# Optimization experiments

Hardware: AMD Instinct MI355X
Metric: run time of the kernel (lower is better)

## Reference

```python
import jax, jax.numpy as jnp
import numpy as np

B, S, H = 2, 2048, 2048
NH, HD = 16, 128


def rotate_half(x):
    x1, x2 = x[..., : x.shape[-1] // 2], x[..., x.shape[-1] // 2 :]
    return jnp.concatenate((-x2, x1), axis=-1)


def setup_inputs() -> dict:
    key = jax.random.key(0)
    ks = jax.random.split(key, 8)
    return {
        "hidden": jax.random.normal(ks[0], (B, S, H), dtype=jnp.float32),
        "cos": jax.random.uniform(ks[1], (S, HD), dtype=jnp.float32),
        "sin": jax.random.uniform(ks[2], (S, HD), dtype=jnp.float32),
        "attention_mask": jnp.zeros((B, 1, S, S), dtype=jnp.float32),
        "Wq": jax.random.normal(ks[3], (H, H), dtype=jnp.float32) * 0.02,
        "Wk": jax.random.normal(ks[4], (H, H), dtype=jnp.float32) * 0.02,
        "Wv": jax.random.normal(ks[5], (H, H), dtype=jnp.float32) * 0.02,
        "Wo": jax.random.normal(ks[6], (H, H), dtype=jnp.float32) * 0.02,
    }


def reference(hidden, cos, sin, attention_mask, Wq, Wk, Wv, Wo):
    b, s, h = hidden.shape
    # torch Linear: y = x @ W.T ; reshape to [B, NH, S, HD]
    def proj(W):
        return (hidden @ W.T).reshape(b, s, NH, HD).transpose(0, 2, 1, 3)

    q, k, v = proj(Wq), proj(Wk), proj(Wv)
    c = cos[None, None, :, :]  # [1,1,S,HD]
    si = sin[None, None, :, :]
    q = q * c + rotate_half(q) * si
    k = k * c + rotate_half(k) * si
    scores = jnp.einsum("bhqd,bhkd->bhqk", q, k) / jnp.sqrt(jnp.float32(HD))
    scores = scores + attention_mask
    attn = jax.nn.softmax(scores.astype(jnp.float32), axis=-1).astype(q.dtype)
    out = jnp.einsum("bhqk,bhkd->bhqd", attn, v)
    out = out.transpose(0, 2, 1, 3).reshape(b, s, h)
    return out @ Wo.T
```

## Files before the change

### kernel.cpp

```cpp
#include <hip/hip_runtime.h>
#include <hip/hip_bf16.h>
#include <math.h>

#define SEQ 2048
#define HID 2048
#define NHEAD 16
#define HDIM 128
#define LDK 4096

typedef __bf16 bf16_t;
typedef __bf16 bf16x2 __attribute__((ext_vector_type(2)));
typedef __bf16 bf16x4_t __attribute__((ext_vector_type(4)));
typedef __bf16 bf16x8 __attribute__((ext_vector_type(8)));
typedef float f32x4 __attribute__((ext_vector_type(4)));
typedef float f32x16 __attribute__((ext_vector_type(16)));
typedef unsigned u32x4 __attribute__((ext_vector_type(4)));

#define MFMA16(a, b, c) __builtin_amdgcn_mfma_f32_16x16x32_bf16(a, b, c, 0, 0, 0)
#define MFMA32(a, b, c) __builtin_amdgcn_mfma_f32_32x32x16_bf16(a, b, c, 0, 0, 0)
#define GLOAD_LDS(g, l) \
  __builtin_amdgcn_global_load_lds((const __attribute__((address_space(1))) void*)(g), \
                                   (__attribute__((address_space(3))) void*)(l), 16, 0, 0)

static __device__ inline unsigned pk2(float lo, float hi) {
  bf16x2 t; t[0] = (bf16_t)lo; t[1] = (bf16_t)hi;
  return __builtin_bit_cast(unsigned, t);
}

__global__ void cast_hidden(const float* __restrict__ in, bf16_t* __restrict__ out) {
  int i = blockIdx.x * 256 + threadIdx.x;
  float4 v = ((const float4*)in)[i];
  bf16x4_t b;
  b[0] = (bf16_t)v.x; b[1] = (bf16_t)v.y; b[2] = (bf16_t)v.z; b[3] = (bf16_t)v.w;
  ((bf16x4_t*)out)[i] = b;
}

__global__ void cast_weights(const float* __restrict__ a, const float* __restrict__ b,
                             const float* __restrict__ c, const float* __restrict__ d,
                             bf16_t* __restrict__ out) {
  const float* srcs[4] = {a, b, c, d};
  const float* src = srcs[blockIdx.y];
  bf16_t* dst = out + (size_t)blockIdx.y * (HID * HID);
  int i = blockIdx.x * 256 + threadIdx.x;
  float4 v = ((const float4*)src)[i];
  bf16x4_t o;
  o[0] = (bf16_t)v.x; o[1] = (bf16_t)v.y; o[2] = (bf16_t)v.z; o[3] = (bf16_t)v.w;
  ((bf16x4_t*)dst)[i] = o;
}

__global__ __launch_bounds__(512, 2) void gemm256(
    const bf16_t* __restrict__ A, const bf16_t* __restrict__ Bw,
    bf16_t* __restrict__ Cb, float* __restrict__ Cf, int M, int N, int K) {
  __shared__ char smem[131072];
  const int tid = threadIdx.x, lane = tid & 63, wid = tid >> 6;
  const int wr = wid >> 2, wc = wid & 3;
  const int lr = lane & 15, lg = lane >> 4;
  const int xcd = blockIdx.x & 7, l = blockIdx.x >> 3;
  const int brow = (xcd >> 2) * 8 + (l >> 2);
  const int bcol = (xcd & 3) * 4 + (l & 3);
  const int NT = K >> 6;

  const bf16_t* Ab = A + (size_t)(brow * 256) * K;
  const bf16_t* Bb = Bw + (size_t)(bcol * 256) * K;

  f32x4 acc[8][4] = {};
  bf16x8 af[4], bfr[4];
  const int swz = (lg ^ ((lr >> 1) & 3)) << 4;

#define STAGE_HALF(t_, op, kh)                                                        \
  {                                                                                   \
    int tt = (t_) < NT ? (t_) : NT - 1;                                               \
    const bf16_t* gsrc = (op) ? Bb : Ab;                                              \
    char* ldst = smem + (tt & 1) * 65536 + (op) * 32768 + (kh) * 16384;               \
    _Pragma("unroll") for (int is = 0; is < 2; ++is) {                                \
      int p = tid + is * 512;                                                         \
      int row = p >> 2, ch = p & 3;                                                   \
      GLOAD_LDS(gsrc + (size_t)row * K + tt * 64 + (kh) * 32 +                        \
                    ((ch ^ ((row >> 1) & 3)) * 8),                                    \
                ldst + p * 16);                                                       \
    }                                                                                 \
  }

#define PHASE(cb, kh, mh, LOADB, STAGECALL, VM)                                       \
  {                                                                                   \
    _Pragma("unroll") for (int mf = 0; mf < 4; ++mf) {                                \
      int row = wr * 128 + (mh) * 64 + mf * 16 + lr;                                  \
      af[mf] = *(const bf16x8*)(smem + (cb) * 65536 + (kh) * 16384 + row * 64 + swz); \
    }                                                                                 \
    if (LOADB) {                                                                      \
      _Pragma("unroll") for (int nf = 0; nf < 4; ++nf) {                              \
        int row = wc * 64 + nf * 16 + lr;                                             \
        bfr[nf] = *(const bf16x8*)(smem + (cb) * 65536 + 32768 + (kh) * 16384 +       \
                                   row * 64 + swz);                                   \
      }                                                                               \
    }                                                                                 \
    STAGECALL;                                                                        \
    __builtin_amdgcn_s_barrier();                                                     \
    asm volatile("s_waitcnt lgkmcnt(0)" ::: "memory");                                \
    __builtin_amdgcn_sched_barrier(0);                                                \
    __builtin_amdgcn_s_setprio(1);                                                    \
    _Pragma("unroll") for (int mf = 0; mf < 4; ++mf)                                  \
      _Pragma("unroll") for (int nf = 0; nf < 4; ++nf)                                \
        acc[(mh) * 4 + mf][nf] = MFMA16(af[mf], bfr[nf], acc[(mh) * 4 + mf][nf]);     \
    __builtin_amdgcn_s_setprio(0);                                                    \
    if (VM) { asm volatile("s_waitcnt vmcnt(6)" ::: "memory"); }                      \
    __builtin_amdgcn_s_barrier();                                                     \
    __builtin_amdgcn_sched_barrier(0);                                                \
  }

  STAGE_HALF(0, 1, 0); STAGE_HALF(0, 0, 0); STAGE_HALF(0, 1, 1); STAGE_HALF(0, 0, 1);
  STAGE_HALF(1, 1, 0); STAGE_HALF(1, 0, 0); STAGE_HALF(1, 1, 1);
  asm volatile("s_waitcnt vmcnt(6)" ::: "memory");
  __builtin_amdgcn_s_barrier();
  __builtin_amdgcn_sched_barrier(0);

  const int NI = NT >> 1;
  for (int i = 0; i < NI; ++i) {
    const int t2 = 2 * i;
    PHASE(0, 0, 0, 1, STAGE_HALF(t2 + 1, 0, 1), 0);
    PHASE(0, 0, 1, 0, STAGE_HALF(t2 + 2, 1, 0), 0);
    PHASE(0, 1, 0, 1, STAGE_HALF(t2 + 2, 0, 0), 0);
    PHASE(0, 1, 1, 0, STAGE_HALF(t2 + 2, 1, 1), 1);
    PHASE(1, 0, 0, 1, STAGE_HALF(t2 + 2, 0, 1), 0);
    PHASE(1, 0, 1, 0, STAGE_HALF(t2 + 3, 1, 0), 0);
    PHASE(1, 1, 0, 1, STAGE_HALF(t2 + 3, 0, 0), 0);
    PHASE(1, 1, 1, 0, STAGE_HALF(t2 + 3, 1, 1), 1);
  }
#undef PHASE
#undef STAGE_HALF

#pragma unroll
  for (int mi = 0; mi < 8; ++mi)
#pragma unroll
    for (int nf = 0; nf < 4; ++nf)
#pragma unroll
      for (int r = 0; r < 4; ++r) {
        int row = brow * 256 + wr * 128 + (mi >> 2) * 64 + (mi & 3) * 16 + lg * 4 + r;
        int col = bcol * 256 + wc * 64 + nf * 16 + lr;
        float v = acc[mi][nf][r];
        if (Cf) Cf[(size_t)row * N + col] = v;
        else    Cb[(size_t)row * N + col] = (bf16_t)v;
      }
}

__global__ __launch_bounds__(256, 3) void gemm_bt(
    const bf16_t* __restrict__ A, const bf16_t* __restrict__ Bw,
    bf16_t* __restrict__ Cb, float* __restrict__ Cf,
    int M, int N, int K) {
  __shared__ bf16_t As[2][128 * 32];
  __shared__ bf16_t Bs[2][128 * 32];
  const int tid = threadIdx.x;
  const int lane = tid & 63, wid = tid >> 6;
  const int wr = wid >> 1, wc = wid & 1;
  const int lr = lane & 15, lg = lane >> 4;
  const int nwg = gridDim.x;
  const int lid = (blockIdx.x & 7) * (nwg >> 3) + (blockIdx.x >> 3);
  const int nbc = N >> 7;
  const int brow = lid / nbc, bcol = lid % nbc;

  f32x4 acc[4][4] = {};
  const int swz = lg ^ ((lr >> 1) & 3);

  const int srow = tid >> 2, sch = tid & 3;
#define GSTAGE(k0, bb)                                                                   \
  {                                                                                      \
    _Pragma("unroll") for (int is = 0; is < 2; ++is) {                                   \
      int row = srow + is * 64;                                                          \
      int g = (sch ^ ((row >> 1) & 3)) * 8;                                              \
      GLOAD_LDS(A + (size_t)(brow * 128 + row) * K + (k0) + g,                           \
                &As[bb][(row * 4 + sch) * 8]);                                           \
      GLOAD_LDS(Bw + (size_t)(bcol * 128 + row) * K + (k0) + g,                          \
                &Bs[bb][(row * 4 + sch) * 8]);                                           \
    }                                                                                    \
  }

  GSTAGE(0, 0);
  __syncthreads();

  const int nt = K / 32;
  for (int t = 0; t < nt; ++t) {
    const int cb = t & 1;
    if (t + 1 < nt) GSTAGE((t + 1) * 32, cb ^ 1);
    bf16x8 af[4], bfr[4];
#pragma unroll
    for (int m = 0; m < 4; ++m)
      af[m] = *(const bf16x8*)(&As[cb][(wr * 64 + m * 16 + lr) * 32 + swz * 8]);
#pragma unroll
    for (int n = 0; n < 4; ++n)
      bfr[n] = *(const bf16x8*)(&Bs[cb][(wc * 64 + n * 16 + lr) * 32 + swz * 8]);
#pragma unroll
    for (int m = 0; m < 4; ++m)
#pragma unroll
      for (int n = 0; n < 4; ++n)
        acc[m][n] = MFMA16(af[m], bfr[n], acc[m][n]);
    __syncthreads();
  }
#undef GSTAGE

#pragma unroll
  for (int m = 0; m < 4; ++m)
#pragma unroll
    for (int n = 0; n < 4; ++n)
#pragma unroll
      for (int r = 0; r < 4; ++r) {
        int row = brow * 128 + wr * 64 + m * 16 + lg * 4 + r;
        int col = bcol * 128 + wc * 64 + n * 16 + lr;
        float v = acc[m][n][r];
        if (Cf) Cf[(size_t)row * N + col] = v;
        else    Cb[(size_t)row * N + col] = (bf16_t)v;
      }
}

__global__ void rope_qk(bf16_t* __restrict__ QK,
                        const float* __restrict__ cost, const float* __restrict__ sint) {
  const float SCALE = 0.08838834764831845f;
  int idx = blockIdx.x * 256 + threadIdx.x;
  int d8 = idx & 7;
  int t = idx >> 3;
  int h = t & 15;
  int row = t >> 4;
  int s = row & (SEQ - 1);
  size_t base = (size_t)row * LDK + h * HDIM;
  const float4* cp = (const float4*)(cost + s * HDIM);
  const float4* sp = (const float4*)(sint + s * HDIM);
  float4 c0a = cp[d8 * 2], c0b = cp[d8 * 2 + 1];
  float4 c1a = cp[16 + d8 * 2], c1b = cp[16 + d8 * 2 + 1];
  float4 s0a = sp[d8 * 2], s0b = sp[d8 * 2 + 1];
  float4 s1a = sp[16 + d8 * 2], s1b = sp[16 + d8 * 2 + 1];
  float c0[8] = {c0a.x, c0a.y, c0a.z, c0a.w, c0b.x, c0b.y, c0b.z, c0b.w};
  float c1[8] = {c1a.x, c1a.y, c1a.z, c1a.w, c1b.x, c1b.y, c1b.z, c1b.w};
  float s0[8] = {s0a.x, s0a.y, s0a.z, s0a.w, s0b.x, s0b.y, s0b.z, s0b.w};
  float s1[8] = {s1a.x, s1a.y, s1a.z, s1a.w, s1b.x, s1b.y, s1b.z, s1b.w};

  bf16_t* Q = QK;
  bf16_t* K = QK + 2048;
  bf16x8 qlo = *(bf16x8*)(Q + base + d8 * 8);
  bf16x8 qhi = *(bf16x8*)(Q + base + 64 + d8 * 8);
  bf16x8 klo = *(bf16x8*)(K + base + d8 * 8);
  bf16x8 khi = *(bf16x8*)(K + base + 64 + d8 * 8);
  bf16x8 qlo2, qhi2, klo2, khi2;
#pragma unroll
  for (int j = 0; j < 8; ++j) {
    float q0 = (float)qlo[j], q1 = (float)qhi[j];
    qlo2[j] = (bf16_t)((q0 * c0[j] - q1 * s0[j]) * SCALE);
    qhi2[j] = (bf16_t)((q1 * c1[j] + q0 * s1[j]) * SCALE);
    float k0 = (float)klo[j], k1 = (float)khi[j];
    klo2[j] = (bf16_t)(k0 * c0[j] - k1 * s0[j]);
    khi2[j] = (bf16_t)(k1 * c1[j] + k0 * s1[j]);
  }
  *(bf16x8*)(Q + base + d8 * 8) = qlo2;
  *(bf16x8*)(Q + base + 64 + d8 * 8) = qhi2;
  *(bf16x8*)(K + base + d8 * 8) = klo2;
  *(bf16x8*)(K + base + 64 + d8 * 8) = khi2;
}

__global__ void transpose_v(const bf16_t* __restrict__ Vf, bf16_t* __restrict__ Vt) {
  __shared__ bf16_t t[32][33];
  int tx = threadIdx.x & 31, ty = threadIdx.x >> 5;
  int r0 = blockIdx.y * 32, c0 = blockIdx.x * 32;
#pragma unroll
  for (int j = 0; j < 4; ++j)
    t[ty + j * 8][tx] = Vf[(size_t)(r0 + ty + j * 8) * HID + c0 + tx];
  __syncthreads();
#pragma unroll
  for (int j = 0; j < 4; ++j) {
    int c = c0 + ty + j * 8;
    int r = r0 + tx;
    int h = c >> 7, d = c & 127, b = r >> 11, s = r & (SEQ - 1);
    Vt[(((size_t)(b * NHEAD + h)) * HDIM + d) * SEQ + s] = t[tx][ty + j * 8];
  }
}

__global__ void mask_t(const float* __restrict__ m, bf16_t* __restrict__ mt) {
  __shared__ float t[32][33];
  int tx = threadIdx.x & 31, ty = threadIdx.x >> 5;
  int r0 = blockIdx.y * 32, c0 = blockIdx.x * 32;
  const float* mb = m + (size_t)blockIdx.z * SEQ * SEQ;
  bf16_t* mtb = mt + (size_t)blockIdx.z * SEQ * SEQ;
#pragma unroll
  for (int j = 0; j < 4; ++j)
    t[ty + j * 8][tx] = mb[(size_t)(r0 + ty + j * 8) * SEQ + c0 + tx];
  __syncthreads();
#pragma unroll
  for (int j = 0; j < 4; ++j)
    mtb[(size_t)(c0 + ty + j * 8) * SEQ + r0 + tx] = (bf16_t)t[tx][ty + j * 8];
}

__global__ __launch_bounds__(512, 2) void flash_fwd(
    const bf16_t* __restrict__ Qf, const bf16_t* __restrict__ Kf,
    const bf16_t* __restrict__ Vt, const bf16_t* __restrict__ maskT,
    bf16_t* __restrict__ AO) {
  __shared__ char smem[131072];
  char* KsB = smem;
  char* VsB = smem + 65536;
  const int tid = threadIdx.x, lane = tid & 63, wid = tid >> 6;
  const int q32 = lane & 31, hi = lane >> 5;

  const int x = blockIdx.x;
  const int bh = x & 31, qt = x >> 5;
  const int b = bh >> 4, h = bh & 15;
  const int qg = qt * 256 + wid * 32 + q32;

  bf16x8 qf[8];
  const bf16_t* qptr = Qf + (size_t)(b * SEQ + qg) * LDK + h * HDIM + hi * 8;
#pragma unroll
  for (int ds = 0; ds < 8; ++ds) qf[ds] = *(const bf16x8*)(qptr + ds * 16);

  const bf16_t* mQ = maskT + (size_t)b * SEQ * SEQ + qg;

  float mrun = -INFINITY, lpart = 0.f;
  f32x16 o[4] = {};

#define STAGE_KV(kt_, bb)                                                                \
  {                                                                                      \
    const int kb0_ = (kt_) * 128;                                                        \
    _Pragma("unroll") for (int is = 0; is < 4; ++is) {                                   \
      int p = tid + is * 512;                                                            \
      int row = p >> 4, ch = p & 15;                                                     \
      int src = (ch * 16) ^ ((row & 7) << 4);                                            \
      GLOAD_LDS((const char*)(Kf + (size_t)(b * SEQ + kb0_ + row) * LDK + h * HDIM) +    \
                    src,                                                                 \
                KsB + (bb) * 32768 + p * 16);                                            \
      GLOAD_LDS((const char*)(Vt + (size_t)(bh * HDIM + row) * SEQ + kb0_) + src,        \
                VsB + (bb) * 32768 + p * 16);                                            \
    }                                                                                    \
  }

  STAGE_KV(0, 0);
  __syncthreads();

  const int NT = SEQ / 128;
  for (int kt = 0; kt < NT; ++kt) {
    const int cur = kt & 1;
    const int kb0 = kt * 128;
    if (kt + 1 < NT) STAGE_KV(kt + 1, cur ^ 1);

#pragma unroll
    for (int kb = 0; kb < 4; ++kb) {
      f32x16 sacc;
#pragma unroll
      for (int r = 0; r < 16; ++r) {
        int key = kb0 + kb * 32 + (r & 3) + 8 * (r >> 2) + 4 * hi;
        sacc[r] = (float)mQ[(size_t)key * SEQ];
      }
#pragma unroll
      for (int ds = 0; ds < 8; ++ds) {
        int row = kb * 32 + q32;
        bf16x8 kfr = *(const bf16x8*)(KsB + cur * 32768 + row * 256 +
                                      ((ds * 32 + hi * 16) ^ ((row & 7) << 4)));
        sacc = MFMA32(kfr, qf[ds], sacc);
      }

      float mx = sacc[0];
#pragma unroll
      for (int r = 1; r < 16; ++r) mx = fmaxf(mx, sacc[r]);
      mx = fmaxf(mx, __shfl_xor(mx, 32, 64));
      if (!__all(mx <= mrun + 8.f)) {
        float mnew = fmaxf(mrun, mx);
        float corr = __expf(mrun - mnew);
        mrun = mnew;
        lpart *= corr;
#pragma unroll
        for (int d0 = 0; d0 < 4; ++d0)
#pragma unroll
          for (int r = 0; r < 16; ++r) o[d0][r] *= corr;
      }

      float p[16];
      float rs = 0.f;
#pragma unroll
      for (int r = 0; r < 16; ++r) {
        p[r] = __expf(sacc[r] - mrun);
        rs += p[r];
      }
      lpart += rs;

#pragma unroll
      for (int s = 0; s < 2; ++s) {
        unsigned A1 = pk2(p[8 * s + 0], p[8 * s + 1]);
        unsigned A2 = pk2(p[8 * s + 2], p[8 * s + 3]);
        unsigned B1 = pk2(p[8 * s + 4], p[8 * s + 5]);
        unsigned B2 = pk2(p[8 * s + 6], p[8 * s + 7]);
        unsigned A1s = __shfl_xor(A1, 32, 64);
        unsigned A2s = __shfl_xor(A2, 32, 64);
        unsigned B1s = __shfl_xor(B1, 32, 64);
        unsigned B2s = __shfl_xor(B2, 32, 64);
        unsigned w0 = hi ? B1s : A1;
        unsigned w1 = hi ? B2s : A2;
        unsigned w2 = hi ? B1 : A1s;
        unsigned w3 = hi ? B2 : A2s;
        u32x4 W = {w0, w1, w2, w3};
        bf16x8 pav = __builtin_bit_cast(bf16x8, W);
        const int gs = kb * 2 + s;
#pragma unroll
        for (int d0 = 0; d0 < 4; ++d0) {
          int vrow = d0 * 32 + q32;
          bf16x8 vf = *(const bf16x8*)(VsB + cur * 32768 + vrow * 256 +
                                       ((gs * 32 + hi * 16) ^ ((vrow & 7) << 4)));
          o[d0] = MFMA32(vf, pav, o[d0]);
        }
      }
    }
    __syncthreads();
  }
#undef STAGE_KV

  float l = lpart + __shfl_xor(lpart, 32, 64);
  float rl = 1.f / l;
  bf16_t* aorow = AO + (size_t)(b * SEQ + qg) * HID + h * HDIM;
#pragma unroll
  for (int d0 = 0; d0 < 4; ++d0)
#pragma unroll
    for (int g = 0; g < 4; ++g) {
      unsigned lo = pk2(o[d0][4 * g + 0] * rl, o[d0][4 * g + 1] * rl);
      unsigned hi2 = pk2(o[d0][4 * g + 2] * rl, o[d0][4 * g + 3] * rl);
      int d = d0 * 32 + 8 * g + 4 * hi;
      *(unsigned*)(aorow + d) = lo;
      *(unsigned*)(aorow + d + 2) = hi2;
    }
}

extern "C" void kernel_launch(void* const* d_in, const int* in_sizes, int n_in,
                              void* d_out, int out_size, void* d_ws, size_t ws_size,
                              hipStream_t stream) {
  const float* hidden = (const float*)d_in[0];
  const float* cost   = (const float*)d_in[1];
  const float* sint   = (const float*)d_in[2];
  const float* mask   = (const float*)d_in[3];
  const float* Wq     = (const float*)d_in[4];
  const float* Wk     = (const float*)d_in[5];
  const float* Wv     = (const float*)d_in[6];
  const float* Wo     = (const float*)d_in[7];
  float* out = (float*)d_out;
  char* ws = (char*)d_ws;

  bf16_t* Af    = (bf16_t*)(ws + 0);
  bf16_t* Wqb   = (bf16_t*)(ws + 16777216);
  bf16_t* Wvb   = (bf16_t*)(ws + 33554432);
  bf16_t* Wob   = (bf16_t*)(ws + 41943040);
  bf16_t* QK    = (bf16_t*)(ws + 50331648);
  bf16_t* Vf    = (bf16_t*)(ws + 83886080);
  bf16_t* Vt    = (bf16_t*)(ws + 0);
  bf16_t* maskT = (bf16_t*)(ws + 83886080);
  bf16_t* AO    = (bf16_t*)(ws + 16777216);

  cast_hidden<<<8192, 256, 0, stream>>>(hidden, Af);
  cast_weights<<<dim3(4096, 4), 256, 0, stream>>>(Wq, Wk, Wv, Wo, Wqb);

  gemm256<<<256, 512, 0, stream>>>(Af, Wqb, QK, nullptr, 4096, LDK, HID);
  gemm_bt<<<512, 256, 0, stream>>>(Af, Wvb, Vf, nullptr, 4096, HID, HID);

  rope_qk<<<2048, 256, 0, stream>>>(QK, cost, sint);
  transpose_v<<<dim3(64, 128), 256, 0, stream>>>(Vf, Vt);
  mask_t<<<dim3(64, 64, 2), 256, 0, stream>>>(mask, maskT);

  flash_fwd<<<256, 512, 0, stream>>>(QK, QK + 2048, Vt, maskT, AO);

  gemm_bt<<<512, 256, 0, stream>>>(AO, Wob, nullptr, out, 4096, HID, HID);
}
```

Measured before the change: 319.0 us.

## Pack mask into MFMA-fragment layout and shrink flash tiles to 128x64

Replaces the transposed mask with a packed layout that matches the MFMA accumulator fragment, so each lane loads its 16 mask values as two contiguous 16-byte vectors instead of 16 strided scalar loads. The flash kernel moves to 256-thread blocks covering 128 queries with 64-key tiles and half the LDS, doubling the grid to 512 blocks for better occupancy and CU coverage. Max and sum reductions are rewritten as trees to shorten dependency chains. Smaller key tiles mean more barriers and more K/V staging rounds per block.

```diff
diff --git a/kernel.cpp b/kernel.cpp
--- a/kernel.cpp
+++ b/kernel.cpp
@@ -271,89 +271,103 @@
   }
 }
 
-__global__ void mask_t(const float* __restrict__ m, bf16_t* __restrict__ mt) {
+__global__ void mask_pack(const float* __restrict__ m, bf16_t* __restrict__ mp) {
   __shared__ float t[32][33];
   int tx = threadIdx.x & 31, ty = threadIdx.x >> 5;
-  int r0 = blockIdx.y * 32, c0 = blockIdx.x * 32;
+  int q0 = blockIdx.x * 32, k0 = blockIdx.y * 32;
   const float* mb = m + (size_t)blockIdx.z * SEQ * SEQ;
-  bf16_t* mtb = mt + (size_t)blockIdx.z * SEQ * SEQ;
 #pragma unroll
   for (int j = 0; j < 4; ++j)
-    t[ty + j * 8][tx] = mb[(size_t)(r0 + ty + j * 8) * SEQ + c0 + tx];
+    t[ty + j * 8][tx] = mb[(size_t)(q0 + ty + j * 8) * SEQ + k0 + tx];
   __syncthreads();
-#pragma unroll
-  for (int j = 0; j < 4; ++j)
-    mtb[(size_t)(c0 + ty + j * 8) * SEQ + r0 + tx] = (bf16_t)t[tx][ty + j * 8];
-}
-
-__global__ __launch_bounds__(512, 2) void flash_fwd(
+  int r = tx & 15, hi = tx >> 4;
+  int kl = (r & 3) + 8 * (r >> 2) + 4 * hi;
+  bf16_t* ob = mp + ((size_t)(blockIdx.z * 64 + blockIdx.y) * 2048 + q0) * 32;
+#pragma unroll
+  for (int j = 0; j < 4; ++j) {
+    int qloc = ty + j * 8;
+    ob[(size_t)qloc * 32 + tx] = (bf16_t)t[qloc][kl];
+  }
+}
+
+__global__ __launch_bounds__(256, 2) void flash_fwd(
     const bf16_t* __restrict__ Qf, const bf16_t* __restrict__ Kf,
-    const bf16_t* __restrict__ Vt, const bf16_t* __restrict__ maskT,
+    const bf16_t* __restrict__ Vt, const bf16_t* __restrict__ maskP,
     bf16_t* __restrict__ AO) {
-  __shared__ char smem[131072];
+  __shared__ char smem[65536];
   char* KsB = smem;
-  char* VsB = smem + 65536;
+  char* VsB = smem + 32768;
   const int tid = threadIdx.x, lane = tid & 63, wid = tid >> 6;
   const int q32 = lane & 31, hi = lane >> 5;
 
   const int x = blockIdx.x;
   const int bh = x & 31, qt = x >> 5;
   const int b = bh >> 4, h = bh & 15;
-  const int qg = qt * 256 + wid * 32 + q32;
+  const int qg = qt * 128 + wid * 32 + q32;
 
   bf16x8 qf[8];
   const bf16_t* qptr = Qf + (size_t)(b * SEQ + qg) * LDK + h * HDIM + hi * 8;
 #pragma unroll
   for (int ds = 0; ds < 8; ++ds) qf[ds] = *(const bf16x8*)(qptr + ds * 16);
 
-  const bf16_t* mQ = maskT + (size_t)b * SEQ * SEQ + qg;
+  const bf16_t* mQ = maskP + (size_t)b * 64 * 65536 + (size_t)qg * 32 + hi * 16;
 
   float mrun = -INFINITY, lpart = 0.f;
   f32x16 o[4] = {};
 
 #define STAGE_KV(kt_, bb)                                                                \
   {                                                                                      \
-    const int kb0_ = (kt_) * 128;                                                        \
+    const int kb0_ = (kt_) * 64;                                                         \
     _Pragma("unroll") for (int is = 0; is < 4; ++is) {                                   \
-      int p = tid + is * 512;                                                            \
+      int p = tid + is * 256;                                                            \
       int row = p >> 4, ch = p & 15;                                                     \
       int src = (ch * 16) ^ ((row & 7) << 4);                                            \
       GLOAD_LDS((const char*)(Kf + (size_t)(b * SEQ + kb0_ + row) * LDK + h * HDIM) +    \
                     src,                                                                 \
-                KsB + (bb) * 32768 + p * 16);                                            \
-      GLOAD_LDS((const char*)(Vt + (size_t)(bh * HDIM + row) * SEQ + kb0_) + src,        \
-                VsB + (bb) * 32768 + p * 16);                                            \
+                KsB + (bb) * 16384 + p * 16);                                            \
+    }                                                                                    \
+    _Pragma("unroll") for (int is = 0; is < 4; ++is) {                                   \
+      int p = tid + is * 256;                                                            \
+      int vrow = p >> 3, vch = p & 7;                                                    \
+      int vsrc = (vch * 16) ^ ((vrow & 7) << 4);                                         \
+      GLOAD_LDS((const char*)(Vt + (size_t)(bh * HDIM + vrow) * SEQ + kb0_) + vsrc,      \
+                VsB + (bb) * 16384 + p * 16);                                            \
     }                                                                                    \
   }
 
   STAGE_KV(0, 0);
   __syncthreads();
 
-  const int NT = SEQ / 128;
+  const int NT = SEQ / 64;
   for (int kt = 0; kt < NT; ++kt) {
     const int cur = kt & 1;
-    const int kb0 = kt * 128;
     if (kt + 1 < NT) STAGE_KV(kt + 1, cur ^ 1);
 
 #pragma unroll
-    for (int kb = 0; kb < 4; ++kb) {
+    for (int kb = 0; kb < 2; ++kb) {
+      const int kg = kt * 2 + kb;
+      bf16x8 mk0 = *(const bf16x8*)(mQ + (size_t)kg * 65536);
+      bf16x8 mk1 = *(const bf16x8*)(mQ + (size_t)kg * 65536 + 8);
       f32x16 sacc;
 #pragma unroll
-      for (int r = 0; r < 16; ++r) {
-        int key = kb0 + kb * 32 + (r & 3) + 8 * (r >> 2) + 4 * hi;
-        sacc[r] = (float)mQ[(size_t)key * SEQ];
-      }
+      for (int r = 0; r < 8; ++r) sacc[r] = (float)mk0[r];
+#pragma unroll
+      for (int r = 0; r < 8; ++r) sacc[8 + r] = (float)mk1[r];
+
 #pragma unroll
       for (int ds = 0; ds < 8; ++ds) {
         int row = kb * 32 + q32;
-        bf16x8 kfr = *(const bf16x8*)(KsB + cur * 32768 + row * 256 +
+        bf16x8 kfr = *(const bf16x8*)(KsB + cur * 16384 + row * 256 +
                                       ((ds * 32 + hi * 16) ^ ((row & 7) << 4)));
         sacc = MFMA32(kfr, qf[ds], sacc);
       }
 
-      float mx = sacc[0];
-#pragma unroll
-      for (int r = 1; r < 16; ++r) mx = fmaxf(mx, sacc[r]);
+      float a0 = fmaxf(sacc[0], sacc[1]),  a1 = fmaxf(sacc[2], sacc[3]);
+      float a2 = fmaxf(sacc[4], sacc[5]),  a3 = fmaxf(sacc[6], sacc[7]);
+      float a4 = fmaxf(sacc[8], sacc[9]),  a5 = fmaxf(sacc[10], sacc[11]);
+      float a6 = fmaxf(sacc[12], sacc[13]), a7 = fmaxf(sacc[14], sacc[15]);
+      float mx = fmaxf(fmaxf(fmaxf(a0, a1), fmaxf(a2, a3)),
+                       fmaxf(fmaxf(a4, a5), fmaxf(a6, a7)));
       mx = fmaxf(mx, __shfl_xor(mx, 32, 64));
       if (!__all(mx <= mrun + 8.f)) {
         float mnew = fmaxf(mrun, mx);
@@ -367,13 +381,13 @@
       }
 
       float p[16];
-      float rs = 0.f;
-#pragma unroll
-      for (int r = 0; r < 16; ++r) {
-        p[r] = __expf(sacc[r] - mrun);
-        rs += p[r];
-      }
-      lpart += rs;
+#pragma unroll
+      for (int r = 0; r < 16; ++r) p[r] = __expf(sacc[r] - mrun);
+      {
+        float s0 = p[0] + p[1],  s1 = p[2] + p[3],  s2 = p[4] + p[5],  s3 = p[6] + p[7];
+        float s4 = p[8] + p[9],  s5 = p[10] + p[11], s6 = p[12] + p[13], s7 = p[14] + p[15];
+        lpart += ((s0 + s1) + (s2 + s3)) + ((s4 + s5) + (s6 + s7));
+      }
 
 #pragma unroll
       for (int s = 0; s < 2; ++s) {
@@ -395,7 +409,7 @@
 #pragma unroll
         for (int d0 = 0; d0 < 4; ++d0) {
           int vrow = d0 * 32 + q32;
-          bf16x8 vf = *(const bf16x8*)(VsB + cur * 32768 + vrow * 256 +
+          bf16x8 vf = *(const bf16x8*)(VsB + cur * 16384 + vrow * 128 +
                                        ((gs * 32 + hi * 16) ^ ((vrow & 7) << 4)));
           o[d0] = MFMA32(vf, pav, o[d0]);
         }
@@ -441,7 +455,7 @@
   bf16_t* QK    = (bf16_t*)(ws + 50331648);
   bf16_t* Vf    = (bf16_t*)(ws + 83886080);
   bf16_t* Vt    = (bf16_t*)(ws + 0);
-  bf16_t* maskT = (bf16_t*)(ws + 83886080);
+  bf16_t* maskP = (bf16_t*)(ws + 83886080);
   bf16_t* AO    = (bf16_t*)(ws + 16777216);
 
   cast_hidden<<<8192, 256, 0, stream>>>(hidden, Af);
@@ -452,9 +466,9 @@
 
   rope_qk<<<2048, 256, 0, stream>>>(QK, cost, sint);
   transpose_v<<<dim3(64, 128), 256, 0, stream>>>(Vf, Vt);
-  mask_t<<<dim3(64, 64, 2), 256, 0, stream>>>(mask, maskT);
-
-  flash_fwd<<<256, 512, 0, stream>>>(QK, QK + 2048, Vt, maskT, AO);
+  mask_pack<<<dim3(64, 64, 2), 256, 0, stream>>>(mask, maskP);
+
+  flash_fwd<<<512, 256, 0, stream>>>(QK, QK + 2048, Vt, maskP, AO);
 
   gemm_bt<<<512, 256, 0, stream>>>(AO, Wob, nullptr, out, 4096, HID, HID);
 }
```

Result: no change. 321.8 us (+0.9%).

## Process two query tiles per wave and pre-pack mask into MFMA layout

Applied to the files above, without the earlier changes.

The flash attention kernel now uses 256 threads per block, with each wave handling 64 query rows as two 32-row MFMA tiles. Each K and V fragment read from LDS is reused across both tiles, halving LDS reads per MFMA. The mask is repacked by a new kernel into a layout matching the MFMA accumulator, so it loads with vector reads instead of 16 strided scalar loads per tile. The LDS swizzle widens to 16 rows. In exchange, register pressure roughly doubles and occupancy drops to one 4-wave block per CU, which may expose latency.

```diff
diff --git a/kernel.cpp b/kernel.cpp
--- a/kernel.cpp
+++ b/kernel.cpp
@@ -25,6 +25,23 @@
 static __device__ inline unsigned pk2(float lo, float hi) {
   bf16x2 t; t[0] = (bf16_t)lo; t[1] = (bf16_t)hi;
   return __builtin_bit_cast(unsigned, t);
+}
+
+static __device__ inline bf16x8 pack_slice(const float* p, int hi) {
+  unsigned A1 = pk2(p[0], p[1]);
+  unsigned A2 = pk2(p[2], p[3]);
+  unsigned B1 = pk2(p[4], p[5]);
+  unsigned B2 = pk2(p[6], p[7]);
+  unsigned A1s = __shfl_xor(A1, 32, 64);
+  unsigned A2s = __shfl_xor(A2, 32, 64);
+  unsigned B1s = __shfl_xor(B1, 32, 64);
+  unsigned B2s = __shfl_xor(B2, 32, 64);
+  unsigned w0 = hi ? B1s : A1;
+  unsigned w1 = hi ? B2s : A2;
+  unsigned w2 = hi ? B1 : A1s;
+  unsigned w3 = hi ? B2 : A2s;
+  u32x4 W = {w0, w1, w2, w3};
+  return __builtin_bit_cast(bf16x8, W);
 }
 
 __global__ void cast_hidden(const float* __restrict__ in, bf16_t* __restrict__ out) {
@@ -271,24 +288,28 @@
   }
 }
 
-__global__ void mask_t(const float* __restrict__ m, bf16_t* __restrict__ mt) {
+__global__ void mask_pack(const float* __restrict__ m, bf16_t* __restrict__ mp) {
   __shared__ float t[32][33];
   int tx = threadIdx.x & 31, ty = threadIdx.x >> 5;
-  int r0 = blockIdx.y * 32, c0 = blockIdx.x * 32;
+  int q0 = blockIdx.x * 32, k0 = blockIdx.y * 32;
   const float* mb = m + (size_t)blockIdx.z * SEQ * SEQ;
-  bf16_t* mtb = mt + (size_t)blockIdx.z * SEQ * SEQ;
 #pragma unroll
   for (int j = 0; j < 4; ++j)
-    t[ty + j * 8][tx] = mb[(size_t)(r0 + ty + j * 8) * SEQ + c0 + tx];
+    t[ty + j * 8][tx] = mb[(size_t)(q0 + ty + j * 8) * SEQ + k0 + tx];
   __syncthreads();
-#pragma unroll
-  for (int j = 0; j < 4; ++j)
-    mtb[(size_t)(c0 + ty + j * 8) * SEQ + r0 + tx] = (bf16_t)t[tx][ty + j * 8];
-}
-
-__global__ __launch_bounds__(512, 2) void flash_fwd(
+  int r = tx & 15, hi = tx >> 4;
+  int kl = (r & 3) + 8 * (r >> 2) + 4 * hi;
+  bf16_t* ob = mp + ((size_t)(blockIdx.z * 64 + blockIdx.y) * 2048 + q0) * 32;
+#pragma unroll
+  for (int j = 0; j < 4; ++j) {
+    int qloc = ty + j * 8;
+    ob[(size_t)qloc * 32 + tx] = (bf16_t)t[qloc][kl];
+  }
+}
+
+__global__ __launch_bounds__(256, 1) void flash_fwd(
     const bf16_t* __restrict__ Qf, const bf16_t* __restrict__ Kf,
-    const bf16_t* __restrict__ Vt, const bf16_t* __restrict__ maskT,
+    const bf16_t* __restrict__ Vt, const bf16_t* __restrict__ maskP,
     bf16_t* __restrict__ AO) {
   __shared__ char smem[131072];
   char* KsB = smem;
@@ -299,25 +320,31 @@
   const int x = blockIdx.x;
   const int bh = x & 31, qt = x >> 5;
   const int b = bh >> 4, h = bh & 15;
-  const int qg = qt * 256 + wid * 32 + q32;
-
-  bf16x8 qf[8];
-  const bf16_t* qptr = Qf + (size_t)(b * SEQ + qg) * LDK + h * HDIM + hi * 8;
-#pragma unroll
-  for (int ds = 0; ds < 8; ++ds) qf[ds] = *(const bf16x8*)(qptr + ds * 16);
-
-  const bf16_t* mQ = maskT + (size_t)b * SEQ * SEQ + qg;
-
-  float mrun = -INFINITY, lpart = 0.f;
-  f32x16 o[4] = {};
+  const int qg0 = qt * 256 + wid * 64 + q32;
+
+  bf16x8 qf0[8], qf1[8];
+  const bf16_t* qp0 = Qf + (size_t)(b * SEQ + qg0) * LDK + h * HDIM + hi * 8;
+  const bf16_t* qp1 = qp0 + (size_t)32 * LDK;
+#pragma unroll
+  for (int ds = 0; ds < 8; ++ds) {
+    qf0[ds] = *(const bf16x8*)(qp0 + ds * 16);
+    qf1[ds] = *(const bf16x8*)(qp1 + ds * 16);
+  }
+
+  const bf16_t* mQ0 = maskP + (size_t)b * 64 * 65536 + (size_t)qg0 * 32 + hi * 16;
+  const bf16_t* mQ1 = mQ0 + 32 * 32;
+
+  float mrun0 = -INFINITY, lpart0 = 0.f;
+  float mrun1 = -INFINITY, lpart1 = 0.f;
+  f32x16 o0[4] = {}, o1[4] = {};
 
 #define STAGE_KV(kt_, bb)                                                                \
   {                                                                                      \
     const int kb0_ = (kt_) * 128;                                                        \
-    _Pragma("unroll") for (int is = 0; is < 4; ++is) {                                   \
-      int p = tid + is * 512;                                                            \
+    _Pragma("unroll") for (int is = 0; is < 8; ++is) {                                   \
+      int p = tid + is * 256;                                                            \
       int row = p >> 4, ch = p & 15;                                                     \
-      int src = (ch * 16) ^ ((row & 7) << 4);                                            \
+      int src = (ch * 16) ^ ((row & 15) << 4);                                           \
       GLOAD_LDS((const char*)(Kf + (size_t)(b * SEQ + kb0_ + row) * LDK + h * HDIM) +    \
                     src,                                                                 \
                 KsB + (bb) * 32768 + p * 16);                                            \
@@ -332,72 +359,101 @@
   const int NT = SEQ / 128;
   for (int kt = 0; kt < NT; ++kt) {
     const int cur = kt & 1;
-    const int kb0 = kt * 128;
     if (kt + 1 < NT) STAGE_KV(kt + 1, cur ^ 1);
 
 #pragma unroll
     for (int kb = 0; kb < 4; ++kb) {
-      f32x16 sacc;
-#pragma unroll
-      for (int r = 0; r < 16; ++r) {
-        int key = kb0 + kb * 32 + (r & 3) + 8 * (r >> 2) + 4 * hi;
-        sacc[r] = (float)mQ[(size_t)key * SEQ];
-      }
+      const int kg = kt * 4 + kb;
+      bf16x8 mk00 = *(const bf16x8*)(mQ0 + (size_t)kg * 65536);
+      bf16x8 mk01 = *(const bf16x8*)(mQ0 + (size_t)kg * 65536 + 8);
+      bf16x8 mk10 = *(const bf16x8*)(mQ1 + (size_t)kg * 65536);
+      bf16x8 mk11 = *(const bf16x8*)(mQ1 + (size_t)kg * 65536 + 8);
+      f32x16 s0, s1;
+#pragma unroll
+      for (int r = 0; r < 8; ++r) {
+        s0[r] = (float)mk00[r]; s0[8 + r] = (float)mk01[r];
+        s1[r] = (float)mk10[r]; s1[8 + r] = (float)mk11[r];
+      }
+
+      const int krow = kb * 32 + q32;
+      const int kswz = (krow & 15) << 4;
 #pragma unroll
       for (int ds = 0; ds < 8; ++ds) {
-        int row = kb * 32 + q32;
-        bf16x8 kfr = *(const bf16x8*)(KsB + cur * 32768 + row * 256 +
-                                      ((ds * 32 + hi * 16) ^ ((row & 7) << 4)));
-        sacc = MFMA32(kfr, qf[ds], sacc);
-      }
-
-      float mx = sacc[0];
-#pragma unroll
-      for (int r = 1; r < 16; ++r) mx = fmaxf(mx, sacc[r]);
-      mx = fmaxf(mx, __shfl_xor(mx, 32, 64));
-      if (!__all(mx <= mrun + 8.f)) {
-        float mnew = fmaxf(mrun, mx);
-        float corr = __expf(mrun - mnew);
-        mrun = mnew;
-        lpart *= corr;
-#pragma unroll
-        for (int d0 = 0; d0 < 4; ++d0)
-#pragma unroll
-          for (int r = 0; r < 16; ++r) o[d0][r] *= corr;
-      }
-
-      float p[16];
-      float rs = 0.f;
-#pragma unroll
-      for (int r = 0; r < 16; ++r) {
-        p[r] = __expf(sacc[r] - mrun);
-        rs += p[r];
-      }
-      lpart += rs;
-
+        bf16x8 kfr = *(const bf16x8*)(KsB + cur * 32768 + krow * 256 +
+                                      ((ds * 32 + hi * 16) ^ kswz));
+        s0 = MFMA32(kfr, qf0[ds], s0);
+        s1 = MFMA32(kfr, qf1[ds], s1);
+      }
+
+      bf16x8 pav00, pav01, pav10, pav11;
+      {
+        float a0 = fmaxf(fmaxf(s0[0], s0[1]), fmaxf(s0[2], s0[3]));
+        float a1 = fmaxf(fmaxf(s0[4], s0[5]), fmaxf(s0[6], s0[7]));
+        float a2 = fmaxf(fmaxf(s0[8], s0[9]), fmaxf(s0[10], s0[11]));
+        float a3 = fmaxf(fmaxf(s0[12], s0[13]), fmaxf(s0[14], s0[15]));
+        float mx = fmaxf(fmaxf(a0, a1), fmaxf(a2, a3));
+        mx = fmaxf(mx, __shfl_xor(mx, 32, 64));
+        if (!__all(mx <= mrun0 + 8.f)) {
+          float mnew = fmaxf(mrun0, mx);
+          float corr = __expf(mrun0 - mnew);
+          mrun0 = mnew; lpart0 *= corr;
+#pragma unroll
+          for (int d0 = 0; d0 < 4; ++d0)
+#pragma unroll
+            for (int r = 0; r < 16; ++r) o0[d0][r] *= corr;
+        }
+        float p_[16];
+#pragma unroll
+        for (int r = 0; r < 16; ++r) p_[r] = __expf(s0[r] - mrun0);
+        float t0 = (p_[0] + p_[1]) + (p_[2] + p_[3]);
+        float t1 = (p_[4] + p_[5]) + (p_[6] + p_[7]);
+        float t2 = (p_[8] + p_[9]) + (p_[10] + p_[11]);
+        float t3 = (p_[12] + p_[13]) + (p_[14] + p_[15]);
+        lpart0 += (t0 + t1) + (t2 + t3);
+        pav00 = pack_slice(p_, hi);
+        pav01 = pack_slice(p_ + 8, hi);
+      }
+      {
+        float a0 = fmaxf(fmaxf(s1[0], s1[1]), fmaxf(s1[2], s1[3]));
+        float a1 = fmaxf(fmaxf(s1[4], s1[5]), fmaxf(s1[6], s1[7]));
+        float a2 = fmaxf(fmaxf(s1[8], s1[9]), fmaxf(s1[10], s1[11]));
+        float a3 = fmaxf(fmaxf(s1[12], s1[13]), fmaxf(s1[14], s1[15]));
+        float mx = fmaxf(fmaxf(a0, a1), fmaxf(a2, a3));
+        mx = fmaxf(mx, __shfl_xor(mx, 32, 64));
+        if (!__all(mx <= mrun1 + 8.f)) {
+          float mnew = fmaxf(mrun1, mx);
+          float corr = __expf(mrun1 - mnew);
+          mrun1 = mnew; lpart1 *= corr;
+#pragma unroll
+          for (int d0 = 0; d0 < 4; ++d0)
+#pragma unroll
+            for (int r = 0; r < 16; ++r) o1[d0][r] *= corr;
+        }
+        float p_[16];
+#pragma unroll
+        for (int r = 0; r < 16; ++r) p_[r] = __expf(s1[r] - mrun1);
+        float t0 = (p_[0] + p_[1]) + (p_[2] + p_[3]);
+        float t1 = (p_[4] + p_[5]) + (p_[6] + p_[7]);
+        float t2 = (p_[8] + p_[9]) + (p_[10] + p_[11]);
+        float t3 = (p_[12] + p_[13]) + (p_[14] + p_[15]);
+        lpart1 += (t0 + t1) + (t2 + t3);
+        pav10 = pack_slice(p_, hi);
+        pav11 = pack_slice(p_ + 8, hi);
+      }
+
+      const int vswzr = q32;
 #pragma unroll
       for (int s = 0; s < 2; ++s) {
-        unsigned A1 = pk2(p[8 * s + 0], p[8 * s + 1]);
-        unsigned A2 = pk2(p[8 * s + 2], p[8 * s + 3]);
-        unsigned B1 = pk2(p[8 * s + 4], p[8 * s + 5]);
-        unsigned B2 = pk2(p[8 * s + 6], p[8 * s + 7]);
-        unsigned A1s = __shfl_xor(A1, 32, 64);
-        unsigned A2s = __shfl_xor(A2, 32, 64);
-        unsigned B1s = __shfl_xor(B1, 32, 64);
-        unsigned B2s = __shfl_xor(B2, 32, 64);
-        unsigned w0 = hi ? B1s : A1;
-        unsigned w1 = hi ? B2s : A2;
-        unsigned w2 = hi ? B1 : A1s;
-        unsigned w3 = hi ? B2 : A2s;
-        u32x4 W = {w0, w1, w2, w3};
-        bf16x8 pav = __builtin_bit_cast(bf16x8, W);
         const int gs = kb * 2 + s;
+        bf16x8 pa0 = s ? pav01 : pav00;
+        bf16x8 pa1 = s ? pav11 : pav10;
 #pragma unroll
         for (int d0 = 0; d0 < 4; ++d0) {
-          int vrow = d0 * 32 + q32;
+          int vrow = d0 * 32 + vswzr;
           bf16x8 vf = *(const bf16x8*)(VsB + cur * 32768 + vrow * 256 +
-                                       ((gs * 32 + hi * 16) ^ ((vrow & 7) << 4)));
-          o[d0] = MFMA32(vf, pav, o[d0]);
+                                       ((gs * 32 + hi * 16) ^ ((vrow & 15) << 4)));
+          o0[d0] = MFMA32(vf, pa0, o0[d0]);
+          o1[d0] = MFMA32(vf, pa1, o1[d0]);
         }
       }
     }
@@ -405,18 +461,24 @@
   }
 #undef STAGE_KV
 
-  float l = lpart + __shfl_xor(lpart, 32, 64);
-  float rl = 1.f / l;
-  bf16_t* aorow = AO + (size_t)(b * SEQ + qg) * HID + h * HDIM;
+  float l0 = lpart0 + __shfl_xor(lpart0, 32, 64);
+  float l1 = lpart1 + __shfl_xor(lpart1, 32, 64);
+  float rl0 = 1.f / l0, rl1 = 1.f / l1;
+  bf16_t* ao0 = AO + (size_t)(b * SEQ + qg0) * HID + h * HDIM;
+  bf16_t* ao1 = ao0 + (size_t)32 * HID;
 #pragma unroll
   for (int d0 = 0; d0 < 4; ++d0)
 #pragma unroll
     for (int g = 0; g < 4; ++g) {
-      unsigned lo = pk2(o[d0][4 * g + 0] * rl, o[d0][4 * g + 1] * rl);
-      unsigned hi2 = pk2(o[d0][4 * g + 2] * rl, o[d0][4 * g + 3] * rl);
       int d = d0 * 32 + 8 * g + 4 * hi;
-      *(unsigned*)(aorow + d) = lo;
-      *(unsigned*)(aorow + d + 2) = hi2;
+      unsigned lo0 = pk2(o0[d0][4 * g + 0] * rl0, o0[d0][4 * g + 1] * rl0);
+      unsigned hi0 = pk2(o0[d0][4 * g + 2] * rl0, o0[d0][4 * g + 3] * rl0);
+      *(unsigned*)(ao0 + d) = lo0;
+      *(unsigned*)(ao0 + d + 2) = hi0;
+      unsigned lo1 = pk2(o1[d0][4 * g + 0] * rl1, o1[d0][4 * g + 1] * rl1);
+      unsigned hi1 = pk2(o1[d0][4 * g + 2] * rl1, o1[d0][4 * g + 3] * rl1);
+      *(unsigned*)(ao1 + d) = lo1;
+      *(unsigned*)(ao1 + d + 2) = hi1;
     }
 }
 
@@ -441,7 +503,7 @@
   bf16_t* QK    = (bf16_t*)(ws + 50331648);
   bf16_t* Vf    = (bf16_t*)(ws + 83886080);
   bf16_t* Vt    = (bf16_t*)(ws + 0);
-  bf16_t* maskT = (bf16_t*)(ws + 83886080);
+  bf16_t* maskP = (bf16_t*)(ws + 83886080);
   bf16_t* AO    = (bf16_t*)(ws + 16777216);
 
   cast_hidden<<<8192, 256, 0, stream>>>(hidden, Af);
@@ -452,9 +514,9 @@
 
   rope_qk<<<2048, 256, 0, stream>>>(QK, cost, sint);
   transpose_v<<<dim3(64, 128), 256, 0, stream>>>(Vf, Vt);
-  mask_t<<<dim3(64, 64, 2), 256, 0, stream>>>(mask, maskT);
-
-  flash_fwd<<<256, 512, 0, stream>>>(QK, QK + 2048, Vt, maskT, AO);
+  mask_pack<<<dim3(64, 64, 2), 256, 0, stream>>>(mask, maskP);
+
+  flash_fwd<<<256, 256, 0, stream>>>(QK, QK + 2048, Vt, maskP, AO);
 
   gemm_bt<<<512, 256, 0, stream>>>(AO, Wob, nullptr, out, 4096, HID, HID);
 }
```

Measured after the change: 347.2 us. 8.9% more time.

## Pack attention mask in MFMA fragment order and widen LDS swizzle

Applied to the files above, without the earlier changes.

Replaces the transposed bf16 mask with a packed layout in which each lane's 16 mask values for a 32-key block are contiguous. The flash kernel can then read them with two 16-byte loads instead of 16 scalar strided loads. It also widens the K/V LDS XOR swizzle from 8 to 16 rows to cut bank conflicts, and rewrites the max and sum reductions as trees. The new packed layout must exactly match the MFMA accumulator ordering, so any mismatch would silently produce wrong masking.

```diff
diff --git a/kernel.cpp b/kernel.cpp
--- a/kernel.cpp
+++ b/kernel.cpp
@@ -25,6 +25,23 @@
 static __device__ inline unsigned pk2(float lo, float hi) {
   bf16x2 t; t[0] = (bf16_t)lo; t[1] = (bf16_t)hi;
   return __builtin_bit_cast(unsigned, t);
+}
+
+static __device__ inline bf16x8 pack_slice(const float* p, int hi) {
+  unsigned A1 = pk2(p[0], p[1]);
+  unsigned A2 = pk2(p[2], p[3]);
+  unsigned B1 = pk2(p[4], p[5]);
+  unsigned B2 = pk2(p[6], p[7]);
+  unsigned A1s = __shfl_xor(A1, 32, 64);
+  unsigned A2s = __shfl_xor(A2, 32, 64);
+  unsigned B1s = __shfl_xor(B1, 32, 64);
+  unsigned B2s = __shfl_xor(B2, 32, 64);
+  unsigned w0 = hi ? B1s : A1;
+  unsigned w1 = hi ? B2s : A2;
+  unsigned w2 = hi ? B1 : A1s;
+  unsigned w3 = hi ? B2 : A2s;
+  u32x4 W = {w0, w1, w2, w3};
+  return __builtin_bit_cast(bf16x8, W);
 }
 
 __global__ void cast_hidden(const float* __restrict__ in, bf16_t* __restrict__ out) {
@@ -271,24 +288,28 @@
   }
 }
 
-__global__ void mask_t(const float* __restrict__ m, bf16_t* __restrict__ mt) {
+__global__ void mask_pack(const float* __restrict__ m, bf16_t* __restrict__ mp) {
   __shared__ float t[32][33];
   int tx = threadIdx.x & 31, ty = threadIdx.x >> 5;
-  int r0 = blockIdx.y * 32, c0 = blockIdx.x * 32;
+  int q0 = blockIdx.x * 32, k0 = blockIdx.y * 32;
   const float* mb = m + (size_t)blockIdx.z * SEQ * SEQ;
-  bf16_t* mtb = mt + (size_t)blockIdx.z * SEQ * SEQ;
 #pragma unroll
   for (int j = 0; j < 4; ++j)
-    t[ty + j * 8][tx] = mb[(size_t)(r0 + ty + j * 8) * SEQ + c0 + tx];
+    t[ty + j * 8][tx] = mb[(size_t)(q0 + ty + j * 8) * SEQ + k0 + tx];
   __syncthreads();
-#pragma unroll
-  for (int j = 0; j < 4; ++j)
-    mtb[(size_t)(c0 + ty + j * 8) * SEQ + r0 + tx] = (bf16_t)t[tx][ty + j * 8];
+  int r = tx & 15, hi = tx >> 4;
+  int kl = (r & 3) + 8 * (r >> 2) + 4 * hi;
+  bf16_t* ob = mp + ((size_t)(blockIdx.z * 64 + blockIdx.y) * 2048 + q0) * 32;
+#pragma unroll
+  for (int j = 0; j < 4; ++j) {
+    int qloc = ty + j * 8;
+    ob[(size_t)qloc * 32 + tx] = (bf16_t)t[qloc][kl];
+  }
 }
 
 __global__ __launch_bounds__(512, 2) void flash_fwd(
     const bf16_t* __restrict__ Qf, const bf16_t* __restrict__ Kf,
-    const bf16_t* __restrict__ Vt, const bf16_t* __restrict__ maskT,
+    const bf16_t* __restrict__ Vt, const bf16_t* __restrict__ maskP,
     bf16_t* __restrict__ AO) {
   __shared__ char smem[131072];
   char* KsB = smem;
@@ -306,7 +327,7 @@
 #pragma unroll
   for (int ds = 0; ds < 8; ++ds) qf[ds] = *(const bf16x8*)(qptr + ds * 16);
 
-  const bf16_t* mQ = maskT + (size_t)b * SEQ * SEQ + qg;
+  const bf16_t* mQ = maskP + (size_t)b * 64 * 65536 + (size_t)qg * 32 + hi * 16;
 
   float mrun = -INFINITY, lpart = 0.f;
   f32x16 o[4] = {};
@@ -317,7 +338,7 @@
     _Pragma("unroll") for (int is = 0; is < 4; ++is) {                                   \
       int p = tid + is * 512;                                                            \
       int row = p >> 4, ch = p & 15;                                                     \
-      int src = (ch * 16) ^ ((row & 7) << 4);                                            \
+      int src = (ch * 16) ^ ((row & 15) << 4);                                           \
       GLOAD_LDS((const char*)(Kf + (size_t)(b * SEQ + kb0_ + row) * LDK + h * HDIM) +    \
                     src,                                                                 \
                 KsB + (bb) * 32768 + p * 16);                                            \
@@ -332,71 +353,65 @@
   const int NT = SEQ / 128;
   for (int kt = 0; kt < NT; ++kt) {
     const int cur = kt & 1;
-    const int kb0 = kt * 128;
     if (kt + 1 < NT) STAGE_KV(kt + 1, cur ^ 1);
 
 #pragma unroll
     for (int kb = 0; kb < 4; ++kb) {
+      const int kg = kt * 4 + kb;
+      bf16x8 mk0 = *(const bf16x8*)(mQ + (size_t)kg * 65536);
+      bf16x8 mk1 = *(const bf16x8*)(mQ + (size_t)kg * 65536 + 8);
       f32x16 sacc;
 #pragma unroll
-      for (int r = 0; r < 16; ++r) {
-        int key = kb0 + kb * 32 + (r & 3) + 8 * (r >> 2) + 4 * hi;
-        sacc[r] = (float)mQ[(size_t)key * SEQ];
-      }
+      for (int r = 0; r < 8; ++r) {
+        sacc[r] = (float)mk0[r];
+        sacc[8 + r] = (float)mk1[r];
+      }
+
+      const int krow = kb * 32 + q32;
+      const int kswz = (krow & 15) << 4;
 #pragma unroll
       for (int ds = 0; ds < 8; ++ds) {
-        int row = kb * 32 + q32;
-        bf16x8 kfr = *(const bf16x8*)(KsB + cur * 32768 + row * 256 +
-                                      ((ds * 32 + hi * 16) ^ ((row & 7) << 4)));
+        bf16x8 kfr = *(const bf16x8*)(KsB + cur * 32768 + krow * 256 +
+                                      ((ds * 32 + hi * 16) ^ kswz));
         sacc = MFMA32(kfr, qf[ds], sacc);
       }
 
-      float mx = sacc[0];
-#pragma unroll
-      for (int r = 1; r < 16; ++r) mx = fmaxf(mx, sacc[r]);
+      float a0 = fmaxf(fmaxf(sacc[0], sacc[1]), fmaxf(sacc[2], sacc[3]));
+      float a1 = fmaxf(fmaxf(sacc[4], sacc[5]), fmaxf(sacc[6], sacc[7]));
+      float a2 = fmaxf(fmaxf(sacc[8], sacc[9]), fmaxf(sacc[10], sacc[11]));
+      float a3 = fmaxf(fmaxf(sacc[12], sacc[13]), fmaxf(sacc[14], sacc[15]));
+      float mx = fmaxf(fmaxf(a0, a1), fmaxf(a2, a3));
       mx = fmaxf(mx, __shfl_xor(mx, 32, 64));
       if (!__all(mx <= mrun + 8.f)) {
         float mnew = fmaxf(mrun, mx);
         float corr = __expf(mrun - mnew);
-        mrun = mnew;
-        lpart *= corr;
+        mrun = mnew; lpart *= corr;
 #pragma unroll
         for (int d0 = 0; d0 < 4; ++d0)
 #pragma unroll
           for (int r = 0; r < 16; ++r) o[d0][r] *= corr;
       }
 
-      float p[16];
-      float rs = 0.f;
-#pragma unroll
-      for (int r = 0; r < 16; ++r) {
-        p[r] = __expf(sacc[r] - mrun);
-        rs += p[r];
-      }
-      lpart += rs;
+      float p_[16];
+#pragma unroll
+      for (int r = 0; r < 16; ++r) p_[r] = __expf(sacc[r] - mrun);
+      {
+        float t0 = (p_[0] + p_[1]) + (p_[2] + p_[3]);
+        float t1 = (p_[4] + p_[5]) + (p_[6] + p_[7]);
+        float t2 = (p_[8] + p_[9]) + (p_[10] + p_[11]);
+        float t3 = (p_[12] + p_[13]) + (p_[14] + p_[15]);
+        lpart += (t0 + t1) + (t2 + t3);
+      }
 
 #pragma unroll
       for (int s = 0; s < 2; ++s) {
-        unsigned A1 = pk2(p[8 * s + 0], p[8 * s + 1]);
-        unsigned A2 = pk2(p[8 * s + 2], p[8 * s + 3]);
-        unsigned B1 = pk2(p[8 * s + 4], p[8 * s + 5]);
-        unsigned B2 = pk2(p[8 * s + 6], p[8 * s + 7]);
-        unsigned A1s = __shfl_xor(A1, 32, 64);
-        unsigned A2s = __shfl_xor(A2, 32, 64);
-        unsigned B1s = __shfl_xor(B1, 32, 64);
-        unsigned B2s = __shfl_xor(B2, 32, 64);
-        unsigned w0 = hi ? B1s : A1;
-        unsigned w1 = hi ? B2s : A2;
-        unsigned w2 = hi ? B1 : A1s;
-        unsigned w3 = hi ? B2 : A2s;
-        u32x4 W = {w0, w1, w2, w3};
-        bf16x8 pav = __builtin_bit_cast(bf16x8, W);
+        bf16x8 pav = pack_slice(p_ + 8 * s, hi);
         const int gs = kb * 2 + s;
 #pragma unroll
         for (int d0 = 0; d0 < 4; ++d0) {
           int vrow = d0 * 32 + q32;
           bf16x8 vf = *(const bf16x8*)(VsB + cur * 32768 + vrow * 256 +
-                                       ((gs * 32 + hi * 16) ^ ((vrow & 7) << 4)));
+                                       ((gs * 32 + hi * 16) ^ ((vrow & 15) << 4)));
           o[d0] = MFMA32(vf, pav, o[d0]);
         }
       }
@@ -441,7 +456,7 @@
   bf16_t* QK    = (bf16_t*)(ws + 50331648);
   bf16_t* Vf    = (bf16_t*)(ws + 83886080);
   bf16_t* Vt    = (bf16_t*)(ws + 0);
-  bf16_t* maskT = (bf16_t*)(ws + 83886080);
+  bf16_t* maskP = (bf16_t*)(ws + 83886080);
   bf16_t* AO    = (bf16_t*)(ws + 16777216);
 
   cast_hidden<<<8192, 256, 0, stream>>>(hidden, Af);
@@ -452,9 +467,9 @@
 
   rope_qk<<<2048, 256, 0, stream>>>(QK, cost, sint);
   transpose_v<<<dim3(64, 128), 256, 0, stream>>>(Vf, Vt);
-  mask_t<<<dim3(64, 64, 2), 256, 0, stream>>>(mask, maskT);
-
-  flash_fwd<<<256, 512, 0, stream>>>(QK, QK + 2048, Vt, maskT, AO);
+  mask_pack<<<dim3(64, 64, 2), 256, 0, stream>>>(mask, maskP);
+
+  flash_fwd<<<256, 512, 0, stream>>>(QK, QK + 2048, Vt, maskP, AO);
 
   gemm_bt<<<512, 256, 0, stream>>>(AO, Wob, nullptr, out, 4096, HID, HID);
 }
```

Measured after the change: 318.8 us. About the same (-0.1%).
